# Performance work log

Measured on AMD Instinct MI355X. Metric: run time of the kernel, lower is better.

Reference implementation:

```python
import jax, jax.numpy as jnp
import numpy as np

B, N, F = 2, 1024, 128
H1, H2 = 64, 32


def setup_inputs() -> dict:
    key = jax.random.key(0)
    ks = jax.random.split(key, 8)
    x = jax.random.normal(ks[0], (B, N, F), dtype=jnp.float32)
    adj = jax.random.uniform(ks[1], (B, N, N), dtype=jnp.float32)
    mask = jnp.ones((B, N), dtype=bool)
    # torch.nn.Linear default init: U(-1/sqrt(fan_in), 1/sqrt(fan_in))
    s1 = 1.0 / np.sqrt(2 * F)
    s2 = 1.0 / np.sqrt(H1)
    s3 = 1.0 / np.sqrt(H2)
    W1 = jax.random.uniform(ks[2], (2 * F, H1), jnp.float32, -s1, s1)
    b1 = jax.random.uniform(ks[3], (H1,), jnp.float32, -s1, s1)
    W2 = jax.random.uniform(ks[4], (H1, H2), jnp.float32, -s2, s2)
    b2 = jax.random.uniform(ks[5], (H2,), jnp.float32, -s2, s2)
    W3 = jax.random.uniform(ks[6], (H2, 1), jnp.float32, -s3, s3)
    b3 = jax.random.uniform(ks[7], (1,), jnp.float32, -s3, s3)
    return {"x": x, "adj": adj, "mask": mask,
            "W1": W1, "b1": b1, "W2": W2, "b2": b2, "W3": W3, "b3": b3}


def reference(x, adj, mask, W1, b1, W2, b2, W3, b3):
    # Original: edge_pairwise[b,i,j] = concat(x[b,j], x[b,i]) -> MLP -> [B,N,N]
    # Faithful fused form: split W1 rows into the half applied to x_j and the
    # half applied to x_i; first Linear = x@Wj broadcast over i + x@Wi broadcast
    # over j + b1 (identical math, avoids the [B,N,N,2F] concat intermediate).
    f = x.shape[-1]
    Wj, Wi = W1[:f], W1[f:]
    pj = x @ Wj  # [B,N,H1], contribution of x[b,j]
    pi = x @ Wi  # [B,N,H1], contribution of x[b,i]
    h = jax.nn.relu(pj[:, None, :, :] + pi[:, :, None, :] + b1)  # [B,N,N,H1]
    h = jax.nn.relu(h @ W2 + b2)  # [B,N,N,H2]
    out = (h @ W3 + b3)[..., 0]   # [B,N,N]
    return out
```

## Files before the change

kernel.cpp:

```cpp
#include <hip/hip_runtime.h>

#define BB 2
#define NN 1024
#define FF 128
#define H1 64
#define H2 32
#define XPAD 136
#define PAD 72

typedef __attribute__((ext_vector_type(4))) _Float16 half4;
typedef __attribute__((ext_vector_type(8))) _Float16 half8;
typedef __attribute__((ext_vector_type(16))) float f32x16;
typedef __attribute__((ext_vector_type(2))) float f32x2;

__device__ inline half8 addrelu8(half8 a, half8 b) {
    half8 s = a + b;
    const half8 z = {};
    return __builtin_elementwise_max(s, z);
}

__global__ __launch_bounds__(256, 4) void fused_kernel(
    const float* __restrict__ x, const float* __restrict__ W1,
    const float* __restrict__ b1, const float* __restrict__ W2,
    const float* __restrict__ b2, const float* __restrict__ W3,
    const float* __restrict__ b3, float* __restrict__ out)
{
    __shared__ __align__(16) _Float16 xlds[96][XPAD];
    __shared__ __align__(16) _Float16 plds[64][PAD];
    __shared__ __align__(16) _Float16 pjlds[32][PAD];

    const int tid  = threadIdx.x;
    const int lane = tid & 63;
    const int wv   = tid >> 6;
    const int bid  = blockIdx.x;

    const int b   = bid >> 9;
    const int rem = bid & 511;
    const int i0  = (rem >> 5) * 64;
    const int j0  = (rem & 31) * 32;
    const int jn  = lane & 31;
    const int hi  = lane >> 5;
    const int m   = jn;

    {
        const int xb_i = b * NN + i0, xb_j = b * NN + j0 - 64;
        #pragma unroll
        for (int it = 0; it < 12; ++it) {
            const int idx = tid + it * 256;
            const int row = idx >> 5, c4 = (idx & 31) * 4;
            const int gr  = (row < 64 ? xb_i : xb_j) + row;
            const float4 v = *(const float4*)(x + (size_t)gr * FF + c4);
            half4 hv = {(_Float16)v.x, (_Float16)v.y,
                        (_Float16)v.z, (_Float16)v.w};
            *(half4*)&xlds[row][c4] = hv;
        }
    }
    __syncthreads();

    auto gemm_unit = [&](int xrow0, int htile, int koff,
                         _Float16* dstbase, const float* bias) {
        f32x16 acc = {};
        #pragma unroll
        for (int ks = 0; ks < 8; ++ks) {
            const int k0 = ks * 16 + hi * 8;
            half8 af;
            const float* wb = W1 + (size_t)(koff + k0) * H1 + htile * 32 + m;
            #pragma unroll
            for (int e = 0; e < 8; ++e)
                af[e] = (_Float16)wb[(size_t)e * H1];
            const half8 bf = *(const half8*)&xlds[xrow0 + m][k0];
            acc = __builtin_amdgcn_mfma_f32_32x32x16_f16(af, bf, acc, 0, 0, 0);
        }
        _Float16* drow = dstbase + (size_t)m * PAD;
        #pragma unroll
        for (int q = 0; q < 4; ++q) {
            half4 hv;
            #pragma unroll
            for (int jj = 0; jj < 4; ++jj) {
                const int r  = q * 4 + jj;
                const int hg = htile * 32 + 8 * q + 4 * hi + jj;
                float v = acc[r];
                if (bias) v += bias[hg];
                hv[jj] = (_Float16)v;
            }
            *(half4*)(drow + htile * 32 + 8 * q + 4 * hi) = hv;
        }
    };
    if (wv == 0) {
        gemm_unit(0,  0, FF, &plds[0][0],  b1);
        gemm_unit(64, 0, 0,  &pjlds[0][0], nullptr);
    } else if (wv == 1) {
        gemm_unit(0,  1, FF, &plds[0][0],  b1);
        gemm_unit(64, 1, 0,  &pjlds[0][0], nullptr);
    } else if (wv == 2) {
        gemm_unit(32, 0, FF, &plds[32][0], b1);
    } else {
        gemm_unit(32, 1, FF, &plds[32][0], b1);
    }

    half8 wa[4];
    #pragma unroll
    for (int c4 = 0; c4 < 4; ++c4)
        #pragma unroll
        for (int e = 0; e < 8; ++e)
            wa[c4][e] = (_Float16)W2[(16 * c4 + hi * 8 + e) * H2 + jn];

    f32x16 ci;
    #pragma unroll
    for (int r = 0; r < 16; ++r) {
        const int row = (r & 3) + 8 * (r >> 2) + 4 * hi;
        ci[r] = b2[row];
    }
    f32x2 w32[8];
    #pragma unroll
    for (int q = 0; q < 8; ++q) {
        const int row = ((2 * q) & 3) + 8 * (q >> 1) + 4 * hi;
        w32[q] = (f32x2){W3[row], W3[row + 1]};
    }
    const float b3v = b3[0];

    __syncthreads();

    const _Float16* pr = &pjlds[jn][hi * 8];
    const half8 qj0 = *(const half8*)(pr);
    const half8 qj1 = *(const half8*)(pr + 16);
    const half8 qj2 = *(const half8*)(pr + 32);
    const half8 qj3 = *(const half8*)(pr + 48);

    auto epi = [&](const f32x16& dd) -> float {
        const f32x2 z2 = {0.f, 0.f};
        f32x2 s[4] = {z2, z2, z2, z2};
        #pragma unroll
        for (int q = 0; q < 8; ++q) {
            f32x2 dp = {dd[2 * q], dd[2 * q + 1]};
            dp = __builtin_elementwise_max(dp, z2);
            s[q & 3] = __builtin_elementwise_fma(dp, w32[q], s[q & 3]);
        }
        const f32x2 t01 = s[0] + s[1];
        const f32x2 t23 = s[2] + s[3];
        const f32x2 tt  = t01 + t23;
        float p = tt[0] + tt[1];
        p += __shfl_xor(p, 32);
        return p;
    };

    const int srow = wv * 16;
    const _Float16* irbase = &plds[srow][hi * 8];
    float* obase = out + (size_t)(b * NN + i0 + srow) * NN + j0 + jn;

    half8 e0 = addrelu8(qj0, *(const half8*)(irbase));
    half8 e1 = addrelu8(qj1, *(const half8*)(irbase + 16));
    half8 e2 = addrelu8(qj2, *(const half8*)(irbase + 32));
    half8 e3 = addrelu8(qj3, *(const half8*)(irbase + 48));
    f32x16 dP;
    dP = __builtin_amdgcn_mfma_f32_32x32x16_f16(wa[0], e0, ci, 0, 0, 0);
    dP = __builtin_amdgcn_mfma_f32_32x32x16_f16(wa[1], e1, dP, 0, 0, 0);
    dP = __builtin_amdgcn_mfma_f32_32x32x16_f16(wa[2], e2, dP, 0, 0, 0);
    dP = __builtin_amdgcn_mfma_f32_32x32x16_f16(wa[3], e3, dP, 0, 0, 0);
    {
        const _Float16* ir = irbase + PAD;
        e0 = addrelu8(qj0, *(const half8*)(ir));
        e1 = addrelu8(qj1, *(const half8*)(ir + 16));
        e2 = addrelu8(qj2, *(const half8*)(ir + 32));
        e3 = addrelu8(qj3, *(const half8*)(ir + 48));
    }
    float pe = 0.f;

    #pragma unroll 2
    for (int t = 1; t < 16; ++t) {
        const int tn = (t < 15) ? t + 1 : 15;
        const _Float16* ir = irbase + tn * PAD;
        const half8 m0 = *(const half8*)(ir);
        const half8 m1 = *(const half8*)(ir + 16);
        const half8 m2 = *(const half8*)(ir + 32);
        const half8 m3 = *(const half8*)(ir + 48);
        f32x16 d;
        d = __builtin_amdgcn_mfma_f32_32x32x16_f16(wa[0], e0, ci, 0, 0, 0);
        d = __builtin_amdgcn_mfma_f32_32x32x16_f16(wa[1], e1, d,  0, 0, 0);
        d = __builtin_amdgcn_mfma_f32_32x32x16_f16(wa[2], e2, d,  0, 0, 0);
        d = __builtin_amdgcn_mfma_f32_32x32x16_f16(wa[3], e3, d,  0, 0, 0);
        const float p = epi(dP);
        if ((t - 1) & 1) {
            const float v = hi ? p : pe;
            obase[(size_t)(t - 2 + hi) * NN] = v + b3v;
        } else {
            pe = p;
        }
        e0 = addrelu8(qj0, m0);
        e1 = addrelu8(qj1, m1);
        e2 = addrelu8(qj2, m2);
        e3 = addrelu8(qj3, m3);
        dP = d;
    }
    {
        const float p = epi(dP);
        const float v = hi ? p : pe;
        obase[(size_t)(14 + hi) * NN] = v + b3v;
    }
}

extern "C" void kernel_launch(void* const* d_in, const int* in_sizes, int n_in,
                              void* d_out, int out_size, void* d_ws, size_t ws_size,
                              hipStream_t stream) {
    const float* x  = (const float*)d_in[0];
    const float* W1 = (const float*)d_in[3];
    const float* b1 = (const float*)d_in[4];
    const float* W2 = (const float*)d_in[5];
    const float* b2 = (const float*)d_in[6];
    const float* W3 = (const float*)d_in[7];
    const float* b3 = (const float*)d_in[8];
    float* out = (float*)d_out;

    fused_kernel<<<BB * NN / 2, 256, 0, stream>>>(
        x, W1, b1, W2, b2, W3, b3, out);
}
```

Baseline: 24.72 us.

## Enlarge block tile to 64x64 with 8 waves sharing projection work

Each block now covers a 64x64 (i,j) tile with 512 threads instead of a 64x32 tile with 256 threads, which halves the grid. The per-row and per-column first-layer projections are split so that each of the 8 waves computes exactly one GEMM unit, removing the imbalance where two waves did double work. The aim is to cut redundant recomputation of the i-side projection across j-tiles and to balance the prologue. In exchange the block uses more LDS, and the 512-thread launch bound may limit occupancy or raise register pressure.

```diff
diff --git a/kernel.cpp b/kernel.cpp
--- a/kernel.cpp
+++ b/kernel.cpp
@@ -19,25 +19,25 @@
     return __builtin_elementwise_max(s, z);
 }
 
-__global__ __launch_bounds__(256, 4) void fused_kernel(
+__global__ __launch_bounds__(512, 4) void fused_kernel(
     const float* __restrict__ x, const float* __restrict__ W1,
     const float* __restrict__ b1, const float* __restrict__ W2,
     const float* __restrict__ b2, const float* __restrict__ W3,
     const float* __restrict__ b3, float* __restrict__ out)
 {
-    __shared__ __align__(16) _Float16 xlds[96][XPAD];
+    __shared__ __align__(16) _Float16 xlds[128][XPAD];
     __shared__ __align__(16) _Float16 plds[64][PAD];
-    __shared__ __align__(16) _Float16 pjlds[32][PAD];
+    __shared__ __align__(16) _Float16 pjlds[64][PAD];
 
     const int tid  = threadIdx.x;
     const int lane = tid & 63;
     const int wv   = tid >> 6;
     const int bid  = blockIdx.x;
 
-    const int b   = bid >> 9;
-    const int rem = bid & 511;
-    const int i0  = (rem >> 5) * 64;
-    const int j0  = (rem & 31) * 32;
+    const int b   = bid >> 8;
+    const int rem = bid & 255;
+    const int i0  = (rem >> 4) * 64;
+    const int j0  = (rem & 15) * 64;
     const int jn  = lane & 31;
     const int hi  = lane >> 5;
     const int m   = jn;
@@ -45,8 +45,8 @@
     {
         const int xb_i = b * NN + i0, xb_j = b * NN + j0 - 64;
         #pragma unroll
-        for (int it = 0; it < 12; ++it) {
-            const int idx = tid + it * 256;
+        for (int it = 0; it < 8; ++it) {
+            const int idx = tid + it * 512;
             const int row = idx >> 5, c4 = (idx & 31) * 4;
             const int gr  = (row < 64 ? xb_i : xb_j) + row;
             const float4 v = *(const float4*)(x + (size_t)gr * FF + c4);
@@ -57,8 +57,13 @@
     }
     __syncthreads();
 
-    auto gemm_unit = [&](int xrow0, int htile, int koff,
-                         _Float16* dstbase, const float* bias) {
+    {
+        const int xrow0 = ((wv & 2) ? 32 : 0) + ((wv & 4) ? 64 : 0);
+        const int htile = wv & 1;
+        const int koff  = (wv & 4) ? 0 : FF;
+        _Float16* dstbase = (wv & 4) ? &pjlds[xrow0 - 64][0] : &plds[xrow0][0];
+        const float* bias = (wv & 4) ? nullptr : b1;
+
         f32x16 acc = {};
         #pragma unroll
         for (int ks = 0; ks < 8; ++ks) {
@@ -85,17 +90,6 @@
             }
             *(half4*)(drow + htile * 32 + 8 * q + 4 * hi) = hv;
         }
-    };
-    if (wv == 0) {
-        gemm_unit(0,  0, FF, &plds[0][0],  b1);
-        gemm_unit(64, 0, 0,  &pjlds[0][0], nullptr);
-    } else if (wv == 1) {
-        gemm_unit(0,  1, FF, &plds[0][0],  b1);
-        gemm_unit(64, 1, 0,  &pjlds[0][0], nullptr);
-    } else if (wv == 2) {
-        gemm_unit(32, 0, FF, &plds[32][0], b1);
-    } else {
-        gemm_unit(32, 1, FF, &plds[32][0], b1);
     }
 
     half8 wa[4];
@@ -121,7 +115,10 @@
 
     __syncthreads();
 
-    const _Float16* pr = &pjlds[jn][hi * 8];
+    const int rowgrp = wv >> 1;
+    const int jhalf  = wv & 1;
+
+    const _Float16* pr = &pjlds[jhalf * 32 + jn][hi * 8];
     const half8 qj0 = *(const half8*)(pr);
     const half8 qj1 = *(const half8*)(pr + 16);
     const half8 qj2 = *(const half8*)(pr + 32);
@@ -144,9 +141,9 @@
         return p;
     };
 
-    const int srow = wv * 16;
-    const _Float16* irbase = &plds[srow][hi * 8];
-    float* obase = out + (size_t)(b * NN + i0 + srow) * NN + j0 + jn;
+    const _Float16* irbase = &plds[rowgrp * 16][hi * 8];
+    float* obase = out + (size_t)(b * NN + i0 + rowgrp * 16) * NN
+                       + j0 + jhalf * 32 + jn;
 
     half8 e0 = addrelu8(qj0, *(const half8*)(irbase));
     half8 e1 = addrelu8(qj1, *(const half8*)(irbase + 16));
@@ -211,6 +208,6 @@
     const float* b3 = (const float*)d_in[8];
     float* out = (float*)d_out;
 
-    fused_kernel<<<BB * NN / 2, 256, 0, stream>>>(
+    fused_kernel<<<BB * NN * NN / (64 * 64), 512, 0, stream>>>(
         x, W1, b1, W2, b2, W3, b3, out);
 }
```

After: 23.00 us. -7.0%, faster.
